# Kernel optimization log

Measured on AMD Instinct MI355X. Metric: run time of the kernel, lower is better.

## Reference

```python
import jax, jax.numpy as jnp
import numpy as np


def setup_inputs() -> dict:
    key = jax.random.key(0)
    ks = jax.random.split(key, 5)
    B, T, I, H, O = 256, 2048, 256, 256, 16
    x = jax.random.normal(ks[0], (B, T, I), dtype=jnp.float32)
    W_ih = jax.random.normal(ks[1], (I, H), dtype=jnp.float32) * 0.05
    W_hh = jax.random.normal(ks[2], (H, H), dtype=jnp.float32) * 0.05
    b_h = jnp.zeros((H,), dtype=jnp.float32)
    fc_w = jax.random.normal(ks[3], (O, H), dtype=jnp.float32) * 0.05
    fc_b = jnp.zeros((O,), dtype=jnp.float32)
    return {"x": x, "W_ih": W_ih, "W_hh": W_hh, "b_h": b_h, "fc_w": fc_w, "fc_b": fc_b}


def reference(x, W_ih, W_hh, b_h, fc_w, fc_b):
    # x: [B, T, I]. Precompute input projections for all timesteps in one GEMM,
    # then scan the strictly sequential hidden-state recurrence.
    B, T, I = x.shape
    H = W_hh.shape[0]
    xp = jnp.einsum('bti,ih->tbh', x, W_ih) + b_h  # [T, B, H]

    def step(h, xt):
        h = jnp.tanh(xt + h @ W_hh)
        return h, None

    h0 = jnp.zeros((B, H), dtype=x.dtype)
    h_final, _ = jax.lax.scan(step, h0, xp)
    return h_final @ fc_w.T + fc_b  # [B, O]
```

## Files before the change

kernel.cpp:

```cpp
#include <hip/hip_runtime.h>
#include <hip/hip_bf16.h>


typedef _Float16 f16;
typedef _Float16 h8_t __attribute__((ext_vector_type(8)));
typedef _Float16 h2_t __attribute__((ext_vector_type(2)));
typedef float    f4_t __attribute__((ext_vector_type(4)));

__device__ __forceinline__ float fdot2u(unsigned w, unsigned h, float c) {
  return __builtin_amdgcn_fdot2(__builtin_bit_cast(h2_t, w),
                                __builtin_bit_cast(h2_t, h), c, false);
}

__device__ __forceinline__ unsigned pkrtz(float a, float b) {
  return __builtin_bit_cast(unsigned, __builtin_amdgcn_cvt_pkrtz(a, b));
}

__global__ __launch_bounds__(256) void prep_kernel(const float* __restrict__ Wih,
                                                   const float* __restrict__ Whh,
                                                   f16* __restrict__ Wt,
                                                   unsigned* __restrict__ Wc) {
  int idx = blockIdx.x * 256 + threadIdx.x;
  if (idx < 65536) {
    int n = idx >> 8, k = idx & 255;
    Wt[n * 256 + k] = (f16)Wih[k * 256 + n];
  } else {
    int p = idx - 65536;
    int j = p >> 7, pp = p & 127;
    Wc[j * 128 + pp] = pkrtz(Whh[(2 * pp) * 256 + j], Whh[(2 * pp + 1) * 256 + j]);
  }
}

__global__ __launch_bounds__(256, 2) void gemm_kernel(const float* __restrict__ x,
                                                      const f16* __restrict__ Wt,
                                                      f16* __restrict__ xp,
                                                      int t0, int CT) {
  int tid = threadIdx.x;
  int wave = tid >> 6, lane = tid & 63;
  int l15 = lane & 15, q = lane >> 4;

  uint4 bf[4][8];
#pragma unroll
  for (int nt = 0; nt < 4; ++nt) {
    int n = (wave * 4 + nt) * 16 + l15;
    const uint4* bp = (const uint4*)(Wt + (size_t)n * 256 + q * 8);
#pragma unroll
    for (int ks = 0; ks < 8; ++ks) bf[nt][ks] = bp[ks * 4];
  }

  int tiles = CT * 4;
  for (int tile = blockIdx.x; tile < tiles; tile += gridDim.x) {
    int tl = tile >> 2;
    int t = t0 + tl;
    int b0 = (tile & 3) << 6;
    size_t obase = (size_t)tl * 65536;

    for (int mt = 0; mt < 4; ++mt) {
      int row = b0 + mt * 16 + l15;
      const float* xr = x + ((size_t)row * 2048 + t) * 256 + q * 8;
      f4_t acc[4];
#pragma unroll
      for (int nt = 0; nt < 4; ++nt) acc[nt] = (f4_t){0.f, 0.f, 0.f, 0.f};

#pragma unroll
      for (int ks = 0; ks < 8; ++ks) {
        float4 f0 = *(const float4*)(xr + ks * 32);
        float4 f1 = *(const float4*)(xr + ks * 32 + 4);
        uint4 au;
        au.x = pkrtz(f0.x, f0.y);
        au.y = pkrtz(f0.z, f0.w);
        au.z = pkrtz(f1.x, f1.y);
        au.w = pkrtz(f1.z, f1.w);
        h8_t a = __builtin_bit_cast(h8_t, au);
#pragma unroll
        for (int nt = 0; nt < 4; ++nt)
          acc[nt] = __builtin_amdgcn_mfma_f32_16x16x32_f16(
              a, __builtin_bit_cast(h8_t, bf[nt][ks]), acc[nt], 0, 0, 0);
      }
#pragma unroll
      for (int nt = 0; nt < 4; ++nt) {
        int n = (wave * 4 + nt) * 16 + l15;
#pragma unroll
        for (int r = 0; r < 4; ++r) {
          int brow = b0 + mt * 16 + q * 4 + r;
          xp[obase + (size_t)brow * 256 + n] = (f16)acc[nt][r];
        }
      }
    }
  }
}

__global__ __launch_bounds__(256) void rnn_kernel(const f16* __restrict__ xp,
                                                  const unsigned* __restrict__ Wc,
                                                  const float* __restrict__ b_h,
                                                  const float* __restrict__ fc_w,
                                                  const float* __restrict__ fc_b,
                                                  float* __restrict__ hstate,
                                                  float* __restrict__ out,
                                                  int t0, int CT) {
  __shared__ uint4 hls[2][32];
  __shared__ float hf[256];
  __shared__ float prt[16][16];

  int b = blockIdx.x, j = threadIdx.x;

  uint4 wv[32];
  const uint4* wp = (const uint4*)(Wc + (size_t)j * 128);
#pragma unroll
  for (int p = 0; p < 32; ++p) wv[p] = wp[p];

  float hcur = (t0 == 0) ? 0.0f : hstate[b * 256 + j];
  ((f16*)hls[0])[j] = (f16)hcur;
  float bhv = b_h[j];

  const f16* xpb = xp + b * 256 + j;
  float xv = (float)xpb[0];
  float xn = (float)xpb[65536];
  __syncthreads();

  for (int tt = 0; tt < CT; ++tt) {
    int pf = (tt + 2 < CT) ? tt + 2 : CT - 1;
    f16 xf = xpb[(size_t)pf * 65536];

    const uint4* hb = hls[tt & 1];
    float a0 = 0.f, a1 = 0.f, a2 = 0.f, a3 = 0.f;
    float a4 = 0.f, a5 = 0.f, a6 = 0.f, a7 = 0.f;
#pragma unroll
    for (int p = 0; p < 32; p += 2) {
      uint4 hv0 = hb[p];
      uint4 hv1 = hb[p + 1];
      a0 = fdot2u(wv[p].x, hv0.x, a0);
      a1 = fdot2u(wv[p].y, hv0.y, a1);
      a2 = fdot2u(wv[p].z, hv0.z, a2);
      a3 = fdot2u(wv[p].w, hv0.w, a3);
      a4 = fdot2u(wv[p + 1].x, hv1.x, a4);
      a5 = fdot2u(wv[p + 1].y, hv1.y, a5);
      a6 = fdot2u(wv[p + 1].z, hv1.z, a6);
      a7 = fdot2u(wv[p + 1].w, hv1.w, a7);
    }
    float z = (((a0 + a1) + (a2 + a3)) + ((a4 + a5) + (a6 + a7))) + xv + bhv;
    float e = __expf(2.0f * z);
    hcur = 1.0f - 2.0f * __builtin_amdgcn_rcpf(e + 1.0f);
    ((f16*)hls[(tt + 1) & 1])[j] = (f16)hcur;
    xv = xn;
    xn = (float)xf;
    __syncthreads();
  }

  hstate[b * 256 + j] = hcur;

  if (t0 + CT == 2048) {
    hf[j] = hcur;
    __syncthreads();
    int o = j >> 4, s = j & 15;
    const float* fw = fc_w + o * 256 + s * 16;
    float p = 0.f;
#pragma unroll
    for (int i = 0; i < 16; ++i) p += hf[s * 16 + i] * fw[i];
    prt[o][s] = p;
    __syncthreads();
    if (j < 16) {
      float r = fc_b[j];
#pragma unroll
      for (int s2 = 0; s2 < 16; ++s2) r += prt[j][s2];
      out[b * 16 + j] = r;
    }
  }
}

extern "C" void kernel_launch(void* const* d_in, const int* in_sizes, int n_in,
                              void* d_out, int out_size, void* d_ws, size_t ws_size,
                              hipStream_t stream) {
  const float* x   = (const float*)d_in[0];
  const float* Wih = (const float*)d_in[1];
  const float* Whh = (const float*)d_in[2];
  const float* bh  = (const float*)d_in[3];
  const float* fcw = (const float*)d_in[4];
  const float* fcb = (const float*)d_in[5];
  float* out = (float*)d_out;

  char* ws = (char*)d_ws;
  f16*      Wt     = (f16*)ws;
  unsigned* Wc     = (unsigned*)(ws + (128 << 10));
  float*    hstate = (float*)(ws + (256 << 10));
  f16*      xpb    = (f16*)(ws + (512 << 10));

  size_t avail = (ws_size > (size_t)(512 << 10)) ? ws_size - (size_t)(512 << 10) : 0;
  int CT = 2048;
  while (CT > 16 && (size_t)CT * 65536 * 2 > avail) CT >>= 1;

  prep_kernel<<<384, 256, 0, stream>>>(Wih, Whh, Wt, Wc);
  for (int t0 = 0; t0 < 2048; t0 += CT) {
    gemm_kernel<<<512, 256, 0, stream>>>(x, Wt, xpb, t0, CT);
    rnn_kernel<<<256, 256, 0, stream>>>(xpb, Wc, bh, fcw, fcb, hstate, out, t0, CT);
  }
}
```

Measured before the change: 2.144 ms.

## Restructure GEMM tiling, xp layout, and split recurrence dot product across waves

Weights are prepacked into MFMA fragment order so each thread loads its fragments with coalesced uint4 reads. The GEMM now stages contiguous 64-timestep x tiles per batch row in LDS and writes xp batch-major, so the recurrence reads contiguous per-batch rows. The recurrence splits each hidden unit's 256-term dot product across four waves, each owning a 64-wide K slice. Partial sums are reduced through LDS, which adds one extra barrier per timestep in exchange for fewer broadcast LDS reads of h per thread.

```diff
diff --git a/kernel.cpp b/kernel.cpp
--- a/kernel.cpp
+++ b/kernel.cpp
@@ -11,159 +11,185 @@
   return __builtin_amdgcn_fdot2(__builtin_bit_cast(h2_t, w),
                                 __builtin_bit_cast(h2_t, h), c, false);
 }
-
 __device__ __forceinline__ unsigned pkrtz(float a, float b) {
   return __builtin_bit_cast(unsigned, __builtin_amdgcn_cvt_pkrtz(a, b));
 }
 
 __global__ __launch_bounds__(256) void prep_kernel(const float* __restrict__ Wih,
                                                    const float* __restrict__ Whh,
-                                                   f16* __restrict__ Wt,
-                                                   unsigned* __restrict__ Wc) {
+                                                   uint4* __restrict__ Wfrag,
+                                                   uint4* __restrict__ Wc2) {
   int idx = blockIdx.x * 256 + threadIdx.x;
-  if (idx < 65536) {
-    int n = idx >> 8, k = idx & 255;
-    Wt[n * 256 + k] = (f16)Wih[k * 256 + n];
+  int e = idx & 8191;
+  int gi = e >> 8;
+  int lg = e & 255;
+  int w = lg >> 6, l = lg & 63;
+  unsigned r[4];
+  if (idx < 8192) {
+    int nt = gi >> 3, ks = gi & 7;
+    int n = w * 64 + nt * 16 + (l & 15);
+    int k0 = ks * 32 + (l >> 4) * 8;
+#pragma unroll
+    for (int c = 0; c < 4; ++c)
+      r[c] = pkrtz(Wih[(k0 + 2 * c) * 256 + n], Wih[(k0 + 2 * c + 1) * 256 + n]);
+    Wfrag[gi * 256 + lg] = make_uint4(r[0], r[1], r[2], r[3]);
   } else {
-    int p = idx - 65536;
-    int j = p >> 7, pp = p & 127;
-    Wc[j * 128 + pp] = pkrtz(Whh[(2 * pp) * 256 + j], Whh[(2 * pp + 1) * 256 + j]);
+    int oi = gi >> 3, q2 = gi & 7;
+    int j = l + 64 * oi;
+    int kb = 64 * w + 8 * q2;
+#pragma unroll
+    for (int c = 0; c < 4; ++c)
+      r[c] = pkrtz(Whh[(kb + 2 * c) * 256 + j], Whh[(kb + 2 * c + 1) * 256 + j]);
+    Wc2[gi * 256 + lg] = make_uint4(r[0], r[1], r[2], r[3]);
   }
 }
 
 __global__ __launch_bounds__(256, 2) void gemm_kernel(const float* __restrict__ x,
-                                                      const f16* __restrict__ Wt,
+                                                      const uint4* __restrict__ Wfrag,
                                                       f16* __restrict__ xp,
-                                                      int t0, int CT) {
+                                                      int t0, int CT, int tpc) {
+  __shared__ f16 As[64][264];
   int tid = threadIdx.x;
-  int wave = tid >> 6, lane = tid & 63;
-  int l15 = lane & 15, q = lane >> 4;
+  int wave = tid >> 6, l = tid & 63, l15 = l & 15, q = l >> 4;
 
   uint4 bf[4][8];
 #pragma unroll
-  for (int nt = 0; nt < 4; ++nt) {
-    int n = (wave * 4 + nt) * 16 + l15;
-    const uint4* bp = (const uint4*)(Wt + (size_t)n * 256 + q * 8);
-#pragma unroll
-    for (int ks = 0; ks < 8; ++ks) bf[nt][ks] = bp[ks * 4];
-  }
-
-  int tiles = CT * 4;
-  for (int tile = blockIdx.x; tile < tiles; tile += gridDim.x) {
-    int tl = tile >> 2;
-    int t = t0 + tl;
-    int b0 = (tile & 3) << 6;
-    size_t obase = (size_t)tl * 65536;
-
-    for (int mt = 0; mt < 4; ++mt) {
-      int row = b0 + mt * 16 + l15;
-      const float* xr = x + ((size_t)row * 2048 + t) * 256 + q * 8;
-      f4_t acc[4];
-#pragma unroll
-      for (int nt = 0; nt < 4; ++nt) acc[nt] = (f4_t){0.f, 0.f, 0.f, 0.f};
-
-#pragma unroll
-      for (int ks = 0; ks < 8; ++ks) {
-        float4 f0 = *(const float4*)(xr + ks * 32);
-        float4 f1 = *(const float4*)(xr + ks * 32 + 4);
-        uint4 au;
-        au.x = pkrtz(f0.x, f0.y);
-        au.y = pkrtz(f0.z, f0.w);
-        au.z = pkrtz(f1.x, f1.y);
-        au.w = pkrtz(f1.z, f1.w);
-        h8_t a = __builtin_bit_cast(h8_t, au);
-#pragma unroll
-        for (int nt = 0; nt < 4; ++nt)
-          acc[nt] = __builtin_amdgcn_mfma_f32_16x16x32_f16(
-              a, __builtin_bit_cast(h8_t, bf[nt][ks]), acc[nt], 0, 0, 0);
-      }
-#pragma unroll
-      for (int nt = 0; nt < 4; ++nt) {
-        int n = (wave * 4 + nt) * 16 + l15;
-#pragma unroll
-        for (int r = 0; r < 4; ++r) {
-          int brow = b0 + mt * 16 + q * 4 + r;
-          xp[obase + (size_t)brow * 256 + n] = (f16)acc[nt][r];
-        }
-      }
-    }
-  }
-}
-
-__global__ __launch_bounds__(256) void rnn_kernel(const f16* __restrict__ xp,
-                                                  const unsigned* __restrict__ Wc,
-                                                  const float* __restrict__ b_h,
-                                                  const float* __restrict__ fc_w,
-                                                  const float* __restrict__ fc_b,
-                                                  float* __restrict__ hstate,
-                                                  float* __restrict__ out,
-                                                  int t0, int CT) {
-  __shared__ uint4 hls[2][32];
+  for (int nt = 0; nt < 4; ++nt)
+#pragma unroll
+    for (int ks = 0; ks < 8; ++ks)
+      bf[nt][ks] = Wfrag[(nt * 8 + ks) * 256 + tid];
+
+  int blk = blockIdx.x;
+  int b = blk / tpc, tt = blk - b * tpc;
+  int tl0 = tt * 64;
+
+  const uint4* xsrc = (const uint4*)(x + ((size_t)b * 2048 + t0 + tl0) * 256);
+#pragma unroll
+  for (int i = 0; i < 16; ++i) {
+    int fi = i * 256 + tid;
+    float4 f = __builtin_bit_cast(float4, xsrc[fi]);
+    int row = fi >> 6;
+    int k = (fi & 63) * 4;
+    uint2 pv; pv.x = pkrtz(f.x, f.y); pv.y = pkrtz(f.z, f.w);
+    *(uint2*)&As[row][k] = pv;
+  }
+  __syncthreads();
+
+  f4_t acc[4][4];
+#pragma unroll
+  for (int mt = 0; mt < 4; ++mt)
+#pragma unroll
+    for (int nt = 0; nt < 4; ++nt) acc[mt][nt] = (f4_t){0.f, 0.f, 0.f, 0.f};
+
+  for (int mt = 0; mt < 4; ++mt) {
+    uint4 af[8];
+#pragma unroll
+    for (int ks = 0; ks < 8; ++ks)
+      af[ks] = *(const uint4*)&As[mt * 16 + l15][ks * 32 + q * 8];
+#pragma unroll
+    for (int ks = 0; ks < 8; ++ks) {
+      h8_t a = __builtin_bit_cast(h8_t, af[ks]);
+#pragma unroll
+      for (int nt = 0; nt < 4; ++nt)
+        acc[mt][nt] = __builtin_amdgcn_mfma_f32_16x16x32_f16(
+            a, __builtin_bit_cast(h8_t, bf[nt][ks]), acc[mt][nt], 0, 0, 0);
+    }
+  }
+
+  f16* xpo = xp + (size_t)b * CT * 256;
+#pragma unroll
+  for (int mt = 0; mt < 4; ++mt)
+#pragma unroll
+    for (int nt = 0; nt < 4; ++nt) {
+      int n = wave * 64 + nt * 16 + l15;
+#pragma unroll
+      for (int r = 0; r < 4; ++r)
+        xpo[(size_t)(tl0 + mt * 16 + q * 4 + r) * 256 + n] = (f16)acc[mt][nt][r];
+    }
+}
+
+__global__ __launch_bounds__(256, 1) void rnn_kernel(const f16* __restrict__ xp,
+                                                     const uint4* __restrict__ Wc2,
+                                                     const float* __restrict__ b_h,
+                                                     const float* __restrict__ fc_w,
+                                                     const float* __restrict__ fc_b,
+                                                     float* __restrict__ hstate,
+                                                     float* __restrict__ out,
+                                                     int t0, int CT) {
+  __shared__ f16 hbuf[2][256];
+  __shared__ float prt[4][256];
   __shared__ float hf[256];
-  __shared__ float prt[16][16];
-
-  int b = blockIdx.x, j = threadIdx.x;
+  __shared__ float prt2[16][16];
+
+  int b = blockIdx.x, tid = threadIdx.x;
+  int w = tid >> 6, l = tid & 63;
 
   uint4 wv[32];
-  const uint4* wp = (const uint4*)(Wc + (size_t)j * 128);
-#pragma unroll
-  for (int p = 0; p < 32; ++p) wv[p] = wp[p];
-
-  float hcur = (t0 == 0) ? 0.0f : hstate[b * 256 + j];
-  ((f16*)hls[0])[j] = (f16)hcur;
-  float bhv = b_h[j];
-
-  const f16* xpb = xp + b * 256 + j;
+#pragma unroll
+  for (int g = 0; g < 32; ++g) wv[g] = Wc2[g * 256 + tid];
+
+  float hcur = (t0 == 0) ? 0.0f : hstate[b * 256 + tid];
+  hbuf[0][tid] = (f16)hcur;
+  float bhv = b_h[tid];
+
+  const f16* xpb = xp + (size_t)b * CT * 256 + tid;
   float xv = (float)xpb[0];
-  float xn = (float)xpb[65536];
+  float xn = (float)xpb[256];
   __syncthreads();
 
   for (int tt = 0; tt < CT; ++tt) {
     int pf = (tt + 2 < CT) ? tt + 2 : CT - 1;
-    f16 xf = xpb[(size_t)pf * 65536];
-
-    const uint4* hb = hls[tt & 1];
-    float a0 = 0.f, a1 = 0.f, a2 = 0.f, a3 = 0.f;
-    float a4 = 0.f, a5 = 0.f, a6 = 0.f, a7 = 0.f;
-#pragma unroll
-    for (int p = 0; p < 32; p += 2) {
-      uint4 hv0 = hb[p];
-      uint4 hv1 = hb[p + 1];
-      a0 = fdot2u(wv[p].x, hv0.x, a0);
-      a1 = fdot2u(wv[p].y, hv0.y, a1);
-      a2 = fdot2u(wv[p].z, hv0.z, a2);
-      a3 = fdot2u(wv[p].w, hv0.w, a3);
-      a4 = fdot2u(wv[p + 1].x, hv1.x, a4);
-      a5 = fdot2u(wv[p + 1].y, hv1.y, a5);
-      a6 = fdot2u(wv[p + 1].z, hv1.z, a6);
-      a7 = fdot2u(wv[p + 1].w, hv1.w, a7);
-    }
-    float z = (((a0 + a1) + (a2 + a3)) + ((a4 + a5) + (a6 + a7))) + xv + bhv;
+    f16 xf = xpb[(size_t)pf * 256];
+
+    const uint4* hb = (const uint4*)&hbuf[tt & 1][w * 64];
+    uint4 hh[8];
+#pragma unroll
+    for (int q2 = 0; q2 < 8; ++q2) hh[q2] = hb[q2];
+
+    float s[4];
+#pragma unroll
+    for (int oi = 0; oi < 4; ++oi) {
+      float a0 = 0.f, a1 = 0.f;
+#pragma unroll
+      for (int q2 = 0; q2 < 8; ++q2) {
+        uint4 wq = wv[oi * 8 + q2];
+        a0 = fdot2u(wq.x, hh[q2].x, a0);
+        a1 = fdot2u(wq.y, hh[q2].y, a1);
+        a0 = fdot2u(wq.z, hh[q2].z, a0);
+        a1 = fdot2u(wq.w, hh[q2].w, a1);
+      }
+      s[oi] = a0 + a1;
+    }
+#pragma unroll
+    for (int oi = 0; oi < 4; ++oi) prt[w][l + 64 * oi] = s[oi];
+    __syncthreads();
+
+    float z = prt[0][tid] + prt[1][tid] + prt[2][tid] + prt[3][tid] + xv + bhv;
     float e = __expf(2.0f * z);
     hcur = 1.0f - 2.0f * __builtin_amdgcn_rcpf(e + 1.0f);
-    ((f16*)hls[(tt + 1) & 1])[j] = (f16)hcur;
+    hbuf[(tt + 1) & 1][tid] = (f16)hcur;
     xv = xn;
     xn = (float)xf;
     __syncthreads();
   }
 
-  hstate[b * 256 + j] = hcur;
+  hstate[b * 256 + tid] = hcur;
 
   if (t0 + CT == 2048) {
-    hf[j] = hcur;
-    __syncthreads();
-    int o = j >> 4, s = j & 15;
-    const float* fw = fc_w + o * 256 + s * 16;
+    hf[tid] = hcur;
+    __syncthreads();
+    int o = tid >> 4, s2 = tid & 15;
+    const float* fw = fc_w + o * 256 + s2 * 16;
     float p = 0.f;
 #pragma unroll
-    for (int i = 0; i < 16; ++i) p += hf[s * 16 + i] * fw[i];
-    prt[o][s] = p;
-    __syncthreads();
-    if (j < 16) {
-      float r = fc_b[j];
-#pragma unroll
-      for (int s2 = 0; s2 < 16; ++s2) r += prt[j][s2];
-      out[b * 16 + j] = r;
+    for (int i = 0; i < 16; ++i) p += hf[s2 * 16 + i] * fw[i];
+    prt2[o][s2] = p;
+    __syncthreads();
+    if (tid < 16) {
+      float r = fc_b[tid];
+#pragma unroll
+      for (int s3 = 0; s3 < 16; ++s3) r += prt2[tid][s3];
+      out[b * 16 + tid] = r;
     }
   }
 }
@@ -180,18 +206,19 @@
   float* out = (float*)d_out;
 
   char* ws = (char*)d_ws;
-  f16*      Wt     = (f16*)ws;
-  unsigned* Wc     = (unsigned*)(ws + (128 << 10));
-  float*    hstate = (float*)(ws + (256 << 10));
-  f16*      xpb    = (f16*)(ws + (512 << 10));
+  uint4* Wfrag  = (uint4*)ws;
+  uint4* Wc2    = (uint4*)(ws + (128 << 10));
+  float* hstate = (float*)(ws + (256 << 10));
+  f16*   xpb    = (f16*)(ws + (512 << 10));
 
   size_t avail = (ws_size > (size_t)(512 << 10)) ? ws_size - (size_t)(512 << 10) : 0;
   int CT = 2048;
-  while (CT > 16 && (size_t)CT * 65536 * 2 > avail) CT >>= 1;
-
-  prep_kernel<<<384, 256, 0, stream>>>(Wih, Whh, Wt, Wc);
+  while (CT > 64 && (size_t)CT * 131072 > avail) CT >>= 1;
+  int tpc = CT >> 6;
+
+  prep_kernel<<<64, 256, 0, stream>>>(Wih, Whh, Wfrag, Wc2);
   for (int t0 = 0; t0 < 2048; t0 += CT) {
-    gemm_kernel<<<512, 256, 0, stream>>>(x, Wt, xpb, t0, CT);
-    rnn_kernel<<<256, 256, 0, stream>>>(xpb, Wc, bh, fcw, fcb, hstate, out, t0, CT);
-  }
-}
+    gemm_kernel<<<256 * tpc, 256, 0, stream>>>(x, Wfrag, xpb, t0, CT, tpc);
+    rnn_kernel<<<256, 256, 0, stream>>>(xpb, Wc2, bh, fcw, fcb, hstate, out, t0, CT);
+  }
+}
```

After: 1.969 ms. 8.1% less time.
